# Optimization experiments

Measured on AMD Instinct MI355X. Metric: run time of the kernel, lower is better.

## Reference

```python
import jax, jax.numpy as jnp
import numpy as np

BETA = 0.25  # commitment loss weight


def setup_inputs() -> dict:
    key = jax.random.key(0)
    k1, k2 = jax.random.split(key)
    z = jax.random.normal(k1, (16, 64, 32, 32), dtype=jnp.float32)      # [B,C,H,W]
    emb = jax.random.normal(k2, (8192, 64), dtype=jnp.float32)          # [V,C] codebook
    return {"z": z, "emb": emb}


def reference(z, emb):
    b, c, h, w = z.shape
    # [B,C,H,W] -> [N,C] with N = B*H*W (channels-last flatten, as in torch permute+reshape)
    z_flat = jnp.transpose(z, (0, 2, 3, 1)).reshape(-1, c)
    # squared L2 distances to every code: ||z||^2 + ||e||^2 - 2 z.e
    dist = (
        jnp.sum(z_flat * z_flat, axis=1, keepdims=True)
        + jnp.sum(emb * emb, axis=1)
        - 2.0 * (z_flat @ emb.T)
    )  # [N,V]
    idx = jnp.argmin(dist, axis=1)  # [N]
    z_q = emb[idx].reshape(b, h, w, c).transpose(0, 3, 1, 2)  # [B,C,H,W]
    codebook_loss = jnp.mean((z_q - jax.lax.stop_gradient(z)) ** 2)
    commit_loss = jnp.mean((z - jax.lax.stop_gradient(z_q)) ** 2)
    vq_loss = codebook_loss + BETA * commit_loss
    # straight-through estimator
    z_q_st = z + jax.lax.stop_gradient(z_q - z)
    return z_q_st, idx.reshape(b, h, w), vq_loss
```

## Files before the change

kernel.cpp:

```cpp
#include <hip/hip_runtime.h>


typedef _Float16 half8 __attribute__((ext_vector_type(8)));
typedef float f32x4 __attribute__((ext_vector_type(4)));

#define N_PTS 16384
#define SPLITS 8
#define THR 0.08f


__global__ __launch_bounds__(256) void k_pre(const float* __restrict__ emb,
                                             float* __restrict__ h,
                                             unsigned short* __restrict__ e16,
                                             float* __restrict__ embT,
                                             int* __restrict__ cnt) {
  int v = blockIdx.x * 256 + threadIdx.x;
  const float4* e4 = (const float4*)(emb + v * 64);
  float s = 0.f;
  float row[64];
#pragma unroll
  for (int i = 0; i < 16; ++i) {
    float4 a = e4[i];
    row[i * 4 + 0] = a.x; row[i * 4 + 1] = a.y;
    row[i * 4 + 2] = a.z; row[i * 4 + 3] = a.w;
    s += a.x * a.x + a.y * a.y + a.z * a.z + a.w * a.w;
  }
  unsigned short* base = e16 + (v >> 4) * 1024 + (v & 15) * 8;
#pragma unroll
  for (int c8 = 0; c8 < 8; ++c8) {
    half8 o;
#pragma unroll
    for (int j = 0; j < 8; ++j) o[j] = (_Float16)row[c8 * 8 + j];
    *(half8*)(base + (c8 >> 2) * 512 + (c8 & 3) * 128) = o;
  }
#pragma unroll
  for (int c = 0; c < 64; ++c) embT[c * 8192 + v] = row[c];
  h[v] = 0.5f * s;
  if (v == 0) *cnt = 0;
}

__global__ __launch_bounds__(256, 4) void k1_score(
    const float* __restrict__ z, const unsigned short* __restrict__ e16,
    const float* __restrict__ h,
    float* __restrict__ ps, float* __restrict__ pi, float* __restrict__ p2) {
  const int tid = threadIdx.x;
  const int lane = tid & 63;
  const int wid = tid >> 6;
  const int cl = lane & 15;
  const int gq = lane >> 4;
  const int n0 = blockIdx.x * 128 + wid * 32;
  const int split = blockIdx.y;

  const int b = n0 >> 10;
  const int hw0 = n0 & 1023;

  half8 A[2][2];
  {
    const float* zb = z + b * 65536 + hw0 + cl;
#pragma unroll
    for (int pt = 0; pt < 2; ++pt)
#pragma unroll
      for (int H = 0; H < 2; ++H) {
        half8 a;
#pragma unroll
        for (int j = 0; j < 8; ++j)
          a[j] = (_Float16)zb[pt * 16 + (H * 32 + gq * 8 + j) * 1024];
        A[pt][H] = a;
      }
  }

  float s1[2][4], i1f[2][4], s2[2][4];
#pragma unroll
  for (int pt = 0; pt < 2; ++pt)
#pragma unroll
    for (int r = 0; r < 4; ++r) {
      s1[pt][r] = -3.0e38f; i1f[pt][r] = 0.f; s2[pt][r] = -3.0e38f;
    }

  const int vbase = split * 1024;
  const unsigned short* bbase = e16 + vbase * 64 + lane * 8;

#pragma unroll 2
  for (int T = 0; T < 64; ++T) {
    const unsigned short* bp = bbase + T * 1024;
    half8 B0 = *(const half8*)bp;
    half8 B1 = *(const half8*)(bp + 512);
    const int code = vbase + T * 16 + cl;
    const float nhv = -h[code];
    const float vf = (float)code;

#pragma unroll
    for (int pt = 0; pt < 2; ++pt) {
      f32x4 acc;
      acc[0] = nhv; acc[1] = nhv; acc[2] = nhv; acc[3] = nhv;
      acc = __builtin_amdgcn_mfma_f32_16x16x32_f16(A[pt][0], B0, acc, 0, 0, 0);
      acc = __builtin_amdgcn_mfma_f32_16x16x32_f16(A[pt][1], B1, acc, 0, 0, 0);

#pragma unroll
      for (int r = 0; r < 4; ++r) {
        float sc = acc[r];
        s2[pt][r] = __builtin_amdgcn_fmed3f(sc, s1[pt][r], s2[pt][r]);
        bool gt = sc > s1[pt][r];
        i1f[pt][r] = gt ? vf : i1f[pt][r];
        s1[pt][r] = fmaxf(s1[pt][r], sc);
      }
    }
  }

#pragma unroll
  for (int off = 8; off >= 1; off >>= 1) {
#pragma unroll
    for (int pt = 0; pt < 2; ++pt)
#pragma unroll
      for (int r = 0; r < 4; ++r) {
        float os = __shfl_xor(s1[pt][r], off);
        float oi = __shfl_xor(i1f[pt][r], off);
        float o2 = __shfl_xor(s2[pt][r], off);
        s2[pt][r] = fmaxf(fmaxf(s2[pt][r], o2), fminf(s1[pt][r], os));
        bool gt = os > s1[pt][r];
        i1f[pt][r] = gt ? oi : i1f[pt][r];
        s1[pt][r] = fmaxf(s1[pt][r], os);
      }
  }

  if (cl == 0) {
#pragma unroll
    for (int pt = 0; pt < 2; ++pt)
#pragma unroll
      for (int r = 0; r < 4; ++r) {
        int n = n0 + pt * 16 + gq * 4 + r;
        int o = split * N_PTS + n;
        ps[o] = s1[pt][r]; pi[o] = i1f[pt][r]; p2[o] = s2[pt][r];
      }
  }
}

__global__ __launch_bounds__(256) void k2_merge(
    const float* __restrict__ ps, const float* __restrict__ pi,
    const float* __restrict__ p2,
    int* __restrict__ idxf, float* __restrict__ out_idx,
    int* __restrict__ list, int* __restrict__ cnt) {
  int n = blockIdx.x * 256 + threadIdx.x;
  float S1 = ps[n], I1 = pi[n], S2 = p2[n];
#pragma unroll
  for (int s = 1; s < SPLITS; ++s) {
    int o = s * N_PTS + n;
    float a = ps[o], ai = pi[o], a2 = p2[o];
    if (a > S1) { S2 = fmaxf(fmaxf(S2, a2), S1); S1 = a; I1 = ai; }
    else        { S2 = fmaxf(S2, a); }
  }
  idxf[n] = (int)I1;
  out_idx[n] = I1;
  if (S1 - S2 < THR) {
    int p = atomicAdd(cnt, 1);
    list[p] = n;
  }
}

__global__ __launch_bounds__(1024, 4) void k_rescue(
    const float* __restrict__ z, const float* __restrict__ embT,
    const float* __restrict__ h, const int* __restrict__ list,
    const int* __restrict__ cnt,
    int* __restrict__ idxf, float* __restrict__ out_idx) {
  __shared__ float zsT[64][4];
  __shared__ int pn[4];
  __shared__ float rs[16][4], ri[16][4];
  const int tid = threadIdx.x;
  const int lane = tid & 63, wv = tid >> 6;
  const int count = *cnt;

  for (int base = blockIdx.x * 4; base < count; base += gridDim.x * 4) {
    const int P = min(4, count - base);
    __syncthreads();
    if (tid < 4) pn[tid] = list[base + min(tid, P - 1)];
    __syncthreads();
    if (tid < 256) {
      int p = tid >> 6, c = tid & 63;
      int n = pn[p];
      zsT[c][p] = z[(n >> 10) * 65536 + c * 1024 + (n & 1023)];
    }
    __syncthreads();

    float d[32];
#pragma unroll
    for (int i = 0; i < 32; ++i) d[i] = 0.f;

    const float4* eT = (const float4*)embT;
    float4 cur0 = eT[tid];
    float4 cur1 = eT[1024 + tid];

    for (int c = 0; c < 64; ++c) {
      float4 nxt0, nxt1;
      if (c < 63) {
        const float4* rowp = eT + (c + 1) * 2048 + tid;
        nxt0 = rowp[0];
        nxt1 = rowp[1024];
      }
      float4 zp = *(const float4*)&zsT[c][0];
      float ev[8] = {cur0.x, cur0.y, cur0.z, cur0.w,
                     cur1.x, cur1.y, cur1.z, cur1.w};
#pragma unroll
      for (int k = 0; k < 8; ++k) {
        d[k * 4 + 0] = fmaf(ev[k], zp.x, d[k * 4 + 0]);
        d[k * 4 + 1] = fmaf(ev[k], zp.y, d[k * 4 + 1]);
        d[k * 4 + 2] = fmaf(ev[k], zp.z, d[k * 4 + 2]);
        d[k * 4 + 3] = fmaf(ev[k], zp.w, d[k * 4 + 3]);
      }
      if (c < 63) { cur0 = nxt0; cur1 = nxt1; }
    }

    float4 hv0 = *(const float4*)(h + tid * 4);
    float4 hv1 = *(const float4*)(h + 4096 + tid * 4);
    float bs[4], bi[4];
#pragma unroll
    for (int p = 0; p < 4; ++p) { bs[p] = -3.0e38f; bi[p] = 0.f; }
#pragma unroll
    for (int k = 0; k < 8; ++k) {
      float hk = (k == 0) ? hv0.x : (k == 1) ? hv0.y : (k == 2) ? hv0.z :
                 (k == 3) ? hv0.w : (k == 4) ? hv1.x : (k == 5) ? hv1.y :
                 (k == 6) ? hv1.z : hv1.w;
      float cf = (float)((k < 4 ? 0 : 4096) + tid * 4 + (k & 3));
#pragma unroll
      for (int p = 0; p < 4; ++p) {
        float sc = d[k * 4 + p] - hk;
        if (sc > bs[p]) { bs[p] = sc; bi[p] = cf; }
      }
    }

#pragma unroll
    for (int off = 32; off >= 1; off >>= 1) {
#pragma unroll
      for (int p = 0; p < 4; ++p) {
        float os = __shfl_xor(bs[p], off);
        float oi = __shfl_xor(bi[p], off);
        if (os > bs[p] || (os == bs[p] && oi < bi[p])) { bs[p] = os; bi[p] = oi; }
      }
    }
    if (lane == 0)
#pragma unroll
      for (int p = 0; p < 4; ++p) { rs[wv][p] = bs[p]; ri[wv][p] = bi[p]; }
    __syncthreads();
    if (tid < 4) {
      int p = tid;
      float s = rs[0][p], i = ri[0][p];
#pragma unroll
      for (int w = 1; w < 16; ++w) {
        if (rs[w][p] > s || (rs[w][p] == s && ri[w][p] < i)) { s = rs[w][p]; i = ri[w][p]; }
      }
      if (p < P) {
        int n = pn[p];
        idxf[n] = (int)i;
        out_idx[n] = i;
      }
    }
  }
}

__global__ __launch_bounds__(256) void k3_quant(
    const float* __restrict__ z, const float* __restrict__ emb,
    const int* __restrict__ idxf,
    float* __restrict__ out, float* __restrict__ psum) {
  int t = blockIdx.x * 256 + threadIdx.x;
  int g = t * 4;
  int b = g >> 16;
  int c = (g >> 10) & 63;
  int hw = g & 1023;
  int n = (b << 10) | hw;
  float4 zv = *(const float4*)(z + g);
  int4 iv = *(const int4*)(idxf + n);
  float q0 = emb[iv.x * 64 + c];
  float q1 = emb[iv.y * 64 + c];
  float q2 = emb[iv.z * 64 + c];
  float q3 = emb[iv.w * 64 + c];
  float d0 = q0 - zv.x, d1 = q1 - zv.y, d2 = q2 - zv.z, d3 = q3 - zv.w;
  float4 o;
  o.x = zv.x + d0; o.y = zv.y + d1; o.z = zv.z + d2; o.w = zv.w + d3;
  *(float4*)(out + g) = o;
  float val = d0 * d0 + d1 * d1 + d2 * d2 + d3 * d3;
#pragma unroll
  for (int off = 32; off >= 1; off >>= 1) val += __shfl_down(val, off);
  __shared__ float wsum[4];
  int lane = threadIdx.x & 63, wv = threadIdx.x >> 6;
  if (lane == 0) wsum[wv] = val;
  __syncthreads();
  if (threadIdx.x == 0)
    psum[blockIdx.x] = wsum[0] + wsum[1] + wsum[2] + wsum[3];
}

__global__ __launch_bounds__(256) void k4_loss(const float* __restrict__ psum,
                                               float* __restrict__ out_loss) {
  int tid = threadIdx.x;
  float val = psum[tid] + psum[tid + 256] + psum[tid + 512] + psum[tid + 768];
#pragma unroll
  for (int off = 32; off >= 1; off >>= 1) val += __shfl_down(val, off);
  __shared__ float wsum[4];
  int lane = tid & 63, wv = tid >> 6;
  if (lane == 0) wsum[wv] = val;
  __syncthreads();
  if (tid == 0)
    out_loss[0] = 1.25f * (wsum[0] + wsum[1] + wsum[2] + wsum[3]) * (1.0f / 1048576.0f);
}

extern "C" void kernel_launch(void* const* d_in, const int* in_sizes, int n_in,
                              void* d_out, int out_size, void* d_ws, size_t ws_size,
                              hipStream_t stream) {
  const float* z   = (const float*)d_in[0];
  const float* emb = (const float*)d_in[1];
  float* out = (float*)d_out;
  float* ws  = (float*)d_ws;

  float* h   = ws;
  unsigned short* e16 = (unsigned short*)(ws + 8192);
  float* embT = ws + 8192 + 262144;
  float* ps  = embT + 524288;
  float* pi  = ps + SPLITS * N_PTS;
  float* p2  = pi + SPLITS * N_PTS;
  int* idxf  = (int*)(p2 + SPLITS * N_PTS);
  int* list  = idxf + N_PTS;
  int* cnt   = list + N_PTS;
  float* psum = (float*)(cnt + 1);

  float* out_idx  = out + 1048576;
  float* out_loss = out + 1048576 + 16384;

  k_pre<<<32, 256, 0, stream>>>(emb, h, e16, embT, cnt);
  k1_score<<<dim3(128, SPLITS), 256, 0, stream>>>(z, e16, h, ps, pi, p2);
  k2_merge<<<64, 256, 0, stream>>>(ps, pi, p2, idxf, out_idx, list, cnt);
  k_rescue<<<256, 1024, 0, stream>>>(z, embT, h, list, cnt, idxf, out_idx);
  k3_quant<<<1024, 256, 0, stream>>>(z, emb, idxf, out, psum);
  k4_loss<<<1, 256, 0, stream>>>(psum, out_loss);
}
```

Before: 145.2 us.

## Pack code index into score mantissa bits, widen point tiles, stage norms in LDS

Scores now have their low 13 mantissa bits replaced by an inverted code index, so one max/med3 tracks both best score and index and the separate index array and its shuffles go away. Each wave handles 64 points instead of 32, so each codebook fragment is reused across four point tiles. Splits rise to 16, each covering 512 codes. Negated half-norms are precomputed and staged in shared memory. The rescue threshold is widened to cover the precision lost from truncated mantissas, which may send more points to the slower fp32 rescue kernel.

```diff
diff --git a/kernel.cpp b/kernel.cpp
--- a/kernel.cpp
+++ b/kernel.cpp
@@ -5,12 +5,12 @@
 typedef float f32x4 __attribute__((ext_vector_type(4)));
 
 #define N_PTS 16384
-#define SPLITS 8
-#define THR 0.08f
+#define SPLITS 16
+#define THR 0.22f
 
 
 __global__ __launch_bounds__(256) void k_pre(const float* __restrict__ emb,
-                                             float* __restrict__ h,
+                                             float* __restrict__ hneg,
                                              unsigned short* __restrict__ e16,
                                              float* __restrict__ embT,
                                              int* __restrict__ cnt) {
@@ -35,30 +35,35 @@
   }
 #pragma unroll
   for (int c = 0; c < 64; ++c) embT[c * 8192 + v] = row[c];
-  h[v] = 0.5f * s;
+  hneg[v] = -0.5f * s;
   if (v == 0) *cnt = 0;
 }
 
 __global__ __launch_bounds__(256, 4) void k1_score(
     const float* __restrict__ z, const unsigned short* __restrict__ e16,
-    const float* __restrict__ h,
-    float* __restrict__ ps, float* __restrict__ pi, float* __restrict__ p2) {
+    const float* __restrict__ hneg,
+    float* __restrict__ ps, float* __restrict__ p2) {
+  __shared__ float hs[512];
   const int tid = threadIdx.x;
   const int lane = tid & 63;
   const int wid = tid >> 6;
   const int cl = lane & 15;
   const int gq = lane >> 4;
-  const int n0 = blockIdx.x * 128 + wid * 32;
+  const int n0 = blockIdx.x * 256 + wid * 64;
   const int split = blockIdx.y;
+  const int vbase = split * 512;
+
+  *(float2*)&hs[tid * 2] = *(const float2*)(hneg + vbase + tid * 2);
+  __syncthreads();
 
   const int b = n0 >> 10;
   const int hw0 = n0 & 1023;
 
-  half8 A[2][2];
+  half8 A[4][2];
   {
     const float* zb = z + b * 65536 + hw0 + cl;
 #pragma unroll
-    for (int pt = 0; pt < 2; ++pt)
+    for (int pt = 0; pt < 4; ++pt)
 #pragma unroll
       for (int H = 0; H < 2; ++H) {
         half8 a;
@@ -69,88 +74,81 @@
       }
   }
 
-  float s1[2][4], i1f[2][4], s2[2][4];
-#pragma unroll
-  for (int pt = 0; pt < 2; ++pt)
-#pragma unroll
-    for (int r = 0; r < 4; ++r) {
-      s1[pt][r] = -3.0e38f; i1f[pt][r] = 0.f; s2[pt][r] = -3.0e38f;
-    }
-
-  const int vbase = split * 1024;
+  float s1[4][4], s2[4][4];
+#pragma unroll
+  for (int pt = 0; pt < 4; ++pt)
+#pragma unroll
+    for (int r = 0; r < 4; ++r) { s1[pt][r] = -3.0e38f; s2[pt][r] = -3.0e38f; }
+
   const unsigned short* bbase = e16 + vbase * 64 + lane * 8;
+  int idxb = 8191 - (vbase + cl);
 
 #pragma unroll 2
-  for (int T = 0; T < 64; ++T) {
+  for (int T = 0; T < 32; ++T) {
     const unsigned short* bp = bbase + T * 1024;
     half8 B0 = *(const half8*)bp;
     half8 B1 = *(const half8*)(bp + 512);
-    const int code = vbase + T * 16 + cl;
-    const float nhv = -h[code];
-    const float vf = (float)code;
-
-#pragma unroll
-    for (int pt = 0; pt < 2; ++pt) {
-      f32x4 acc;
-      acc[0] = nhv; acc[1] = nhv; acc[2] = nhv; acc[3] = nhv;
-      acc = __builtin_amdgcn_mfma_f32_16x16x32_f16(A[pt][0], B0, acc, 0, 0, 0);
+    const float nh = hs[T * 16 + cl];
+    f32x4 C0;
+    C0[0] = nh; C0[1] = nh; C0[2] = nh; C0[3] = nh;
+
+#pragma unroll
+    for (int pt = 0; pt < 4; ++pt) {
+      f32x4 acc = __builtin_amdgcn_mfma_f32_16x16x32_f16(A[pt][0], B0, C0, 0, 0, 0);
       acc = __builtin_amdgcn_mfma_f32_16x16x32_f16(A[pt][1], B1, acc, 0, 0, 0);
 
 #pragma unroll
       for (int r = 0; r < 4; ++r) {
-        float sc = acc[r];
-        s2[pt][r] = __builtin_amdgcn_fmed3f(sc, s1[pt][r], s2[pt][r]);
-        bool gt = sc > s1[pt][r];
-        i1f[pt][r] = gt ? vf : i1f[pt][r];
-        s1[pt][r] = fmaxf(s1[pt][r], sc);
-      }
-    }
+        unsigned u = (__float_as_uint(acc[r]) & 0xFFFFE000u) | (unsigned)idxb;
+        float p = __uint_as_float(u);
+        s2[pt][r] = __builtin_amdgcn_fmed3f(p, s1[pt][r], s2[pt][r]);
+        s1[pt][r] = fmaxf(s1[pt][r], p);
+      }
+    }
+    idxb -= 16;
   }
 
 #pragma unroll
   for (int off = 8; off >= 1; off >>= 1) {
 #pragma unroll
-    for (int pt = 0; pt < 2; ++pt)
+    for (int pt = 0; pt < 4; ++pt)
 #pragma unroll
       for (int r = 0; r < 4; ++r) {
         float os = __shfl_xor(s1[pt][r], off);
-        float oi = __shfl_xor(i1f[pt][r], off);
         float o2 = __shfl_xor(s2[pt][r], off);
         s2[pt][r] = fmaxf(fmaxf(s2[pt][r], o2), fminf(s1[pt][r], os));
-        bool gt = os > s1[pt][r];
-        i1f[pt][r] = gt ? oi : i1f[pt][r];
         s1[pt][r] = fmaxf(s1[pt][r], os);
       }
   }
 
   if (cl == 0) {
 #pragma unroll
-    for (int pt = 0; pt < 2; ++pt)
+    for (int pt = 0; pt < 4; ++pt)
 #pragma unroll
       for (int r = 0; r < 4; ++r) {
         int n = n0 + pt * 16 + gq * 4 + r;
         int o = split * N_PTS + n;
-        ps[o] = s1[pt][r]; pi[o] = i1f[pt][r]; p2[o] = s2[pt][r];
+        ps[o] = s1[pt][r]; p2[o] = s2[pt][r];
       }
   }
 }
 
 __global__ __launch_bounds__(256) void k2_merge(
-    const float* __restrict__ ps, const float* __restrict__ pi,
-    const float* __restrict__ p2,
+    const float* __restrict__ ps, const float* __restrict__ p2,
     int* __restrict__ idxf, float* __restrict__ out_idx,
     int* __restrict__ list, int* __restrict__ cnt) {
   int n = blockIdx.x * 256 + threadIdx.x;
-  float S1 = ps[n], I1 = pi[n], S2 = p2[n];
+  float S1 = ps[n], S2 = p2[n];
 #pragma unroll
   for (int s = 1; s < SPLITS; ++s) {
     int o = s * N_PTS + n;
-    float a = ps[o], ai = pi[o], a2 = p2[o];
-    if (a > S1) { S2 = fmaxf(fmaxf(S2, a2), S1); S1 = a; I1 = ai; }
+    float a = ps[o], a2 = p2[o];
+    if (a > S1) { S2 = fmaxf(fmaxf(S2, a2), S1); S1 = a; }
     else        { S2 = fmaxf(S2, a); }
   }
-  idxf[n] = (int)I1;
-  out_idx[n] = I1;
+  int I1 = 8191 - (int)(__float_as_uint(S1) & 0x1FFFu);
+  idxf[n] = I1;
+  out_idx[n] = (float)I1;
   if (S1 - S2 < THR) {
     int p = atomicAdd(cnt, 1);
     list[p] = n;
@@ -159,7 +157,7 @@
 
 __global__ __launch_bounds__(1024, 4) void k_rescue(
     const float* __restrict__ z, const float* __restrict__ embT,
-    const float* __restrict__ h, const int* __restrict__ list,
+    const float* __restrict__ hneg, const int* __restrict__ list,
     const int* __restrict__ cnt,
     int* __restrict__ idxf, float* __restrict__ out_idx) {
   __shared__ float zsT[64][4];
@@ -209,8 +207,8 @@
       if (c < 63) { cur0 = nxt0; cur1 = nxt1; }
     }
 
-    float4 hv0 = *(const float4*)(h + tid * 4);
-    float4 hv1 = *(const float4*)(h + 4096 + tid * 4);
+    float4 hv0 = *(const float4*)(hneg + tid * 4);
+    float4 hv1 = *(const float4*)(hneg + 4096 + tid * 4);
     float bs[4], bi[4];
 #pragma unroll
     for (int p = 0; p < 4; ++p) { bs[p] = -3.0e38f; bi[p] = 0.f; }
@@ -222,7 +220,7 @@
       float cf = (float)((k < 4 ? 0 : 4096) + tid * 4 + (k & 3));
 #pragma unroll
       for (int p = 0; p < 4; ++p) {
-        float sc = d[k * 4 + p] - hk;
+        float sc = d[k * 4 + p] + hk;
         if (sc > bs[p]) { bs[p] = sc; bi[p] = cf; }
       }
     }
@@ -309,12 +307,11 @@
   float* out = (float*)d_out;
   float* ws  = (float*)d_ws;
 
-  float* h   = ws;
+  float* hneg = ws;
   unsigned short* e16 = (unsigned short*)(ws + 8192);
   float* embT = ws + 8192 + 262144;
   float* ps  = embT + 524288;
-  float* pi  = ps + SPLITS * N_PTS;
-  float* p2  = pi + SPLITS * N_PTS;
+  float* p2  = ps + SPLITS * N_PTS;
   int* idxf  = (int*)(p2 + SPLITS * N_PTS);
   int* list  = idxf + N_PTS;
   int* cnt   = list + N_PTS;
@@ -323,10 +320,10 @@
   float* out_idx  = out + 1048576;
   float* out_loss = out + 1048576 + 16384;
 
-  k_pre<<<32, 256, 0, stream>>>(emb, h, e16, embT, cnt);
-  k1_score<<<dim3(128, SPLITS), 256, 0, stream>>>(z, e16, h, ps, pi, p2);
-  k2_merge<<<64, 256, 0, stream>>>(ps, pi, p2, idxf, out_idx, list, cnt);
-  k_rescue<<<256, 1024, 0, stream>>>(z, embT, h, list, cnt, idxf, out_idx);
+  k_pre<<<32, 256, 0, stream>>>(emb, hneg, e16, embT, cnt);
+  k1_score<<<dim3(64, SPLITS), 256, 0, stream>>>(z, e16, hneg, ps, p2);
+  k2_merge<<<64, 256, 0, stream>>>(ps, p2, idxf, out_idx, list, cnt);
+  k_rescue<<<256, 1024, 0, stream>>>(z, embT, hneg, list, cnt, idxf, out_idx);
   k3_quant<<<1024, 256, 0, stream>>>(z, emb, idxf, out, psum);
   k4_loss<<<1, 256, 0, stream>>>(psum, out_loss);
 }
```

Result: slower. 166.0 us (+14.3%).
